# Performance work log

Hardware: AMD Instinct MI355X
Metric: run time of the kernel (lower is better)

The kernel has to match this reference:

```python
import jax, jax.numpy as jnp
import numpy as np
from jax import lax

B, N, C = 16, 2048, 128
NPOINT = 512
RADII = (0.1, 0.2, 0.4)
NSAMPLES = (16, 32, 48)
C_IN = C + 3          # use_xyz: relative xyz concatenated to features
C_OUT = 128
C_MID = C_OUT // 4    # mapping_func1 out channels (non-first-layer)


def fps(xyz, npoint):
    # sequential furthest point sampling; first index is 0 (matches CUDA FPS)
    b, n, _ = xyz.shape
    def step(carry, _):
        dist, last = carry
        p = xyz[jnp.arange(b), last]                    # (B,3) last selected point
        d = jnp.sum((xyz - p[:, None, :]) ** 2, -1)     # (B,N)
        dist = jnp.minimum(dist, d)
        nxt = jnp.argmax(dist, -1).astype(jnp.int32)
        return (dist, nxt), nxt
    idx0 = jnp.zeros((b,), jnp.int32)
    (_, _), rest = lax.scan(step, (jnp.full((b, n), 1e10, jnp.float32), idx0), None, length=npoint - 1)
    return jnp.concatenate([idx0[None], rest], 0).T     # (B,npoint)


def ball_query(xyz, new_xyz, radius, nsample):
    # first `nsample` in-ball indices (in original point order), pad with first hit
    n = xyz.shape[1]
    d2 = jnp.sum((new_xyz[:, :, None, :] - xyz[:, None, :, :]) ** 2, -1)  # (B,np,N)
    scores = jnp.where(d2 < radius * radius, jnp.arange(n, dtype=jnp.int32), n)
    vals = -lax.top_k(-scores, nsample)[0]               # ascending valid indices, invalid == n
    first = vals[..., :1]                                # center is always in its own ball
    return jnp.where(vals >= n, first, vals)             # (B,np,ns) int32


def gather_points(pts, idx):
    # pts (B,N,D), idx (B,np,ns) -> (B,np,ns,D)
    return jax.vmap(lambda p, i: p[i])(pts, idx)


def sa_forward(xyz, features, W1, b1, W2, b2, Wcr, bcr):
    fi = fps(xyz, NPOINT)
    new_xyz = jax.vmap(lambda p, i: p[i])(xyz, fi)       # (B,np,3)
    featT = jnp.transpose(features, (0, 2, 1))           # (B,N,C)
    outs = []
    for r, ns in zip(RADII, NSAMPLES):
        idx = ball_query(xyz, new_xyz, r, ns)
        g_xyz = gather_points(xyz, idx)                  # (B,np,ns,3) absolute neighbor coords
        rel = g_xyz - new_xyz[:, :, None, :]             # relative coords
        gf = gather_points(featT, idx)                   # (B,np,ns,C)
        x = jnp.concatenate([rel, gf], -1)               # (B,np,ns,C_in)
        dist = jnp.linalg.norm(rel, axis=-1, keepdims=True)
        ci = jnp.broadcast_to(new_xyz[:, :, None, :], g_xyz.shape)
        h10 = jnp.concatenate([dist, ci, g_xyz, rel], -1)        # relation prior (B,np,ns,10)
        h = jax.nn.relu(h10 @ W1 + b1) @ W2 + b2                 # dynamic weights (B,np,ns,C_in)
        pooled = jnp.max(jax.nn.relu(h * x), 2)                  # (B,np,C_in) max over neighbors
        outs.append(jax.nn.relu(pooled @ Wcr + bcr))             # channel raising (B,np,C_out)
    new_features = jnp.transpose(jnp.concatenate(outs, -1), (0, 2, 1))  # (B, 3*C_out, np)
    return new_xyz, new_features


def setup_inputs() -> dict:
    key = jax.random.key(0)
    ks = jax.random.split(key, 6)
    s = 0.05
    xyz = jax.random.uniform(ks[0], (B, N, 3), jnp.float32)
    features = jax.random.normal(ks[1], (B, C, N), jnp.float32)
    W1 = jax.random.normal(ks[2], (10, C_MID), jnp.float32) * s
    b1 = jnp.zeros((C_MID,), jnp.float32)
    W2 = jax.random.normal(ks[3], (C_MID, C_IN), jnp.float32) * s
    b2 = jnp.zeros((C_IN,), jnp.float32)
    Wcr = jax.random.normal(ks[4], (C_IN, C_OUT), jnp.float32) * s
    bcr = jnp.zeros((C_OUT,), jnp.float32)
    return dict(xyz=xyz, features=features, W1=W1, b1=b1, W2=W2, b2=b2, Wcr=Wcr, bcr=bcr)


def reference(xyz, features, W1, b1, W2, b2, Wcr, bcr):
    return sa_forward(xyz, features, W1, b1, W2, b2, Wcr, bcr)
```

## Files before the change

kernel.cpp:

```cpp
#include <hip/hip_runtime.h>
#include <hip/hip_bf16.h>

#define BATCH   16
#define NPTS    2048
#define NPOINT  512
#define CFEAT   128
#define CIN     131
#define CMID    32
#define NS_TOT  96

typedef float v2f __attribute__((ext_vector_type(2)));

__device__ __forceinline__ float d2_rn(float ax, float ay, float az,
                                       float bx, float by, float bz) {
  float dx = __fsub_rn(ax, bx), dy = __fsub_rn(ay, by), dz = __fsub_rn(az, bz);
  return __fadd_rn(__fadd_rn(__fmul_rn(dx, dx), __fmul_rn(dy, dy)), __fmul_rn(dz, dz));
}

__device__ __forceinline__ unsigned long long wave_kmax64(unsigned long long k) {
#define KSTEP(CTRL, RMASK, BMASK)                                              \
  {                                                                            \
    unsigned hi = (unsigned)(k >> 32), lo = (unsigned)k;                       \
    unsigned thi = (unsigned)__builtin_amdgcn_update_dpp(                      \
        (int)hi, (int)hi, CTRL, RMASK, BMASK, false);                          \
    unsigned tlo = (unsigned)__builtin_amdgcn_update_dpp(                      \
        (int)lo, (int)lo, CTRL, RMASK, BMASK, false);                          \
    unsigned long long tk = ((unsigned long long)thi << 32) | tlo;             \
    k = tk > k ? tk : k;                                                       \
  }
  KSTEP(0x111, 0xf, 0xf)
  KSTEP(0x112, 0xf, 0xf)
  KSTEP(0x114, 0xf, 0xe)
  KSTEP(0x118, 0xf, 0xc)
  KSTEP(0x142, 0xa, 0xf)
  KSTEP(0x143, 0xc, 0xf)
#undef KSTEP
  return k;
}

__global__ __launch_bounds__(256) void fps_transpose_kernel(
    const float* __restrict__ xyz, const float* __restrict__ feat,
    float* __restrict__ featT, float* __restrict__ out_xyz)
{
  int t = threadIdx.x;
  if (blockIdx.x >= BATCH) {
    __shared__ float tile[32][33];
    int m  = blockIdx.x - BATCH;
    int b  = m >> 8;
    int c0 = ((m >> 6) & 3) << 5;
    int n0 = (m & 63) << 5;
    int tx = t & 31, ty = t >> 5;
    const float* src = feat  + (size_t)b * CFEAT * NPTS;
    float*       dst = featT + (size_t)b * NPTS * CFEAT;
#pragma unroll
    for (int i = 0; i < 4; ++i)
      tile[ty + 8 * i][tx] = src[(size_t)(c0 + ty + 8 * i) * NPTS + n0 + tx];
    __syncthreads();
#pragma unroll
    for (int i = 0; i < 4; ++i)
      dst[(size_t)(n0 + ty + 8 * i) * CFEAT + c0 + tx] = tile[tx][ty + 8 * i];
    return;
  }
  __shared__ float4 sp[NPTS];
  __shared__ unsigned long long skey[2][4];
  __shared__ int slast[NPOINT];
  int b = blockIdx.x;
  const float* xb = xyz + (size_t)b * NPTS * 3;
  for (int n = t; n < NPTS; n += 256) {
    const float* p = xb + n * 3;
    sp[n] = make_float4(p[0], p[1], p[2], 0.f);
  }
  if (t == 0) slast[0] = 0;
  __syncthreads();
  float lx[8], ly[8], lz[8], d[8];
#pragma unroll
  for (int i = 0; i < 8; ++i) {
    float4 q = sp[(i << 8) + t];
    lx[i] = q.x; ly[i] = q.y; lz[i] = q.z;
    d[i] = 1e10f;
  }
  int last = 0;
  int w = t >> 6;
  int tb = 0xFFF - t;
#pragma unroll 1
  for (int step = 1; step < NPOINT; ++step) {
    float4 pv = sp[last];
    unsigned long long best = 0ull;
#pragma unroll
    for (int i = 0; i < 8; ++i) {
      float dd = d2_rn(lx[i], ly[i], lz[i], pv.x, pv.y, pv.z);
      float nd = fminf(d[i], dd);
      d[i] = nd;
      unsigned long long k = ((unsigned long long)__float_as_uint(nd) << 32)
                           | (unsigned)(tb - (i << 8));
      best = (k > best) ? k : best;
    }
    unsigned long long wk = wave_kmax64(best);
    int par = step & 1;
    if ((t & 63) == 63) skey[par][w] = wk;
    __syncthreads();
    unsigned long long k0 = skey[par][0], k1 = skey[par][1];
    unsigned long long k2 = skey[par][2], k3 = skey[par][3];
    unsigned long long ka = k0 > k1 ? k0 : k1;
    unsigned long long kb = k2 > k3 ? k2 : k3;
    unsigned long long km = ka > kb ? ka : kb;
    last = (0xFFF - (int)((unsigned)km & 0xFFFu)) & (NPTS - 1);
    if (t == 0) slast[step] = last;
  }
  __syncthreads();
  for (int s = t; s < NPOINT; s += 256) {
    float4 q = sp[slast[s]];
    float* o = out_xyz + ((size_t)b * NPOINT + s) * 3;
    o[0] = q.x; o[1] = q.y; o[2] = q.z;
  }
}

__global__ __launch_bounds__(128, 4) void center_kernel(
    const float* __restrict__ xyz, const float* __restrict__ featT,
    const float* __restrict__ W1, const float* __restrict__ b1,
    const float* __restrict__ W2, const float* __restrict__ b2,
    const float* __restrict__ Wcr, const float* __restrict__ bcr,
    const float* __restrict__ new_xyz, float* __restrict__ out_feat,
    float* __restrict__ out_tmp)
{
  int j = blockIdx.x, b = blockIdx.y, t = threadIdx.x;
  __shared__ int   sIdx[NS_TOT];
  __shared__ __align__(16) float sH1[NS_TOT * 36];
  __shared__ float sVr[NS_TOT * 4];
  __shared__ __align__(16) float sPooled[3 * 132];

  float cx = new_xyz[((size_t)b * NPOINT + j) * 3 + 0];
  float cy = new_xyz[((size_t)b * NPOINT + j) * 3 + 1];
  float cz = new_xyz[((size_t)b * NPOINT + j) * 3 + 2];

  {
    int w = t >> 6, lane = t & 63;
    const float* xb = xyz + (size_t)b * NPTS * 3;
    unsigned long long lt = (1ull << lane) - 1ull;
    if (w == 0) {
      int c0 = 0, c1 = 0;
      for (int it = 0; it < 32; ++it) {
        int n = (it << 6) + lane;
        float px = xb[n * 3 + 0], py = xb[n * 3 + 1], pz = xb[n * 3 + 2];
        float d2 = d2_rn(cx, cy, cz, px, py, pz);
        bool i0 = d2 < 0.01f, i1 = d2 < 0.04f;
        unsigned long long m0 = __ballot(i0), m1 = __ballot(i1);
        if (i0) { int pos = c0 + __popcll(m0 & lt); if (pos < 16) sIdx[pos] = n; }
        if (i1) { int pos = c1 + __popcll(m1 & lt); if (pos < 32) sIdx[16 + pos] = n; }
        c0 += __popcll(m0); c1 += __popcll(m1);
        if (c0 >= 16 && c1 >= 32) break;
      }
      int f0 = sIdx[0];
      int f1 = sIdx[16];
      if (lane >= c0 && lane < 16) sIdx[lane] = f0;
      if (lane >= c1 && lane < 32) sIdx[16 + lane] = f1;
    } else {
      int c2 = 0;
      for (int it = 0; it < 32; ++it) {
        int n = (it << 6) + lane;
        float px = xb[n * 3 + 0], py = xb[n * 3 + 1], pz = xb[n * 3 + 2];
        float d2 = d2_rn(cx, cy, cz, px, py, pz);
        bool i2 = d2 < 0.16f;
        unsigned long long m2 = __ballot(i2);
        if (i2) { int pos = c2 + __popcll(m2 & lt); if (pos < 48) sIdx[48 + pos] = n; }
        c2 += __popcll(m2);
        if (c2 >= 48) break;
      }
      int f2 = sIdx[48];
      if (lane >= c2 && lane < 48) sIdx[48 + lane] = f2;
    }
  }
  __syncthreads();

  if (t < NS_TOT) {
    int idx = sIdx[t];
    const float* p = xyz + ((size_t)b * NPTS + (size_t)idx) * 3;
    float px = p[0], py = p[1], pz = p[2];
    float rx = __fsub_rn(px, cx), ry = __fsub_rn(py, cy), rz = __fsub_rn(pz, cz);
    float dist = sqrtf(__fadd_rn(__fadd_rn(__fmul_rn(rx, rx), __fmul_rn(ry, ry)),
                                 __fmul_rn(rz, rz)));
    float h10[10] = {dist, cx, cy, cz, px, py, pz, rx, ry, rz};
    float h1r[CMID];
#pragma unroll
    for (int m = 0; m < CMID / 2; ++m) {
      v2f a = { b1[2 * m], b1[2 * m + 1] };
#pragma unroll
      for (int i = 0; i < 10; ++i) {
        v2f wv = { W1[i * CMID + 2 * m], W1[i * CMID + 2 * m + 1] };
        v2f hv = { h10[i], h10[i] };
        a = __builtin_elementwise_fma(hv, wv, a);
      }
      v2f z = { 0.f, 0.f };
      a = __builtin_elementwise_max(a, z);
      h1r[2 * m] = a.x; h1r[2 * m + 1] = a.y;
    }
#pragma unroll
    for (int q = 0; q < 8; ++q)
      *(float4*)&sH1[t * 36 + 4 * q] = *(const float4*)&h1r[4 * q];
    v2f pa0 = { b2[0], 0.f }, pa1 = { b2[1], 0.f }, pa2 = { b2[2], 0.f };
#pragma unroll
    for (int m = 0; m < CMID / 2; ++m) {
      v2f hv = { h1r[2 * m], h1r[2 * m + 1] };
      v2f w0 = { W2[(2 * m) * CIN + 0], W2[(2 * m + 1) * CIN + 0] };
      v2f w1 = { W2[(2 * m) * CIN + 1], W2[(2 * m + 1) * CIN + 1] };
      v2f w2 = { W2[(2 * m) * CIN + 2], W2[(2 * m + 1) * CIN + 2] };
      pa0 = __builtin_elementwise_fma(hv, w0, pa0);
      pa1 = __builtin_elementwise_fma(hv, w1, pa1);
      pa2 = __builtin_elementwise_fma(hv, w2, pa2);
    }
    float a0 = __fadd_rn(pa0.x, pa0.y);
    float a1 = __fadd_rn(pa1.x, pa1.y);
    float a2 = __fadd_rn(pa2.x, pa2.y);
    sVr[t * 4 + 0] = fmaxf(__fmul_rn(a0, rx), 0.f);
    sVr[t * 4 + 1] = fmaxf(__fmul_rn(a1, ry), 0.f);
    sVr[t * 4 + 2] = fmaxf(__fmul_rn(a2, rz), 0.f);
  }
  __syncthreads();

  {
    int w = t >> 6, lane = t & 63;
    v2f wA[16], wB[16];
#pragma unroll
    for (int m = 0; m < 16; ++m) {
      wA[m] = (v2f){ W2[(2 * m) * CIN + 3 + lane],
                     W2[(2 * m + 1) * CIN + 3 + lane] };
      wB[m] = (v2f){ W2[(2 * m) * CIN + 3 + lane + 64],
                     W2[(2 * m + 1) * CIN + 3 + lane + 64] };
    }
    float bA = b2[3 + lane], bB = b2[3 + lane + 64];
    const float* ftb = featT + (size_t)b * NPTS * CFEAT;
    int sBeg = w ? 48 : 0;
    int sEnd = w ? 96 : 48;
    int sMid = w ? 10000 : 16;
    float xA0 = ftb[(size_t)sIdx[sBeg] * CFEAT + lane];
    float xB0 = ftb[(size_t)sIdx[sBeg] * CFEAT + lane + 64];
    float xA1 = ftb[(size_t)sIdx[sBeg + 1] * CFEAT + lane];
    float xB1 = ftb[(size_t)sIdx[sBeg + 1] * CFEAT + lane + 64];
    float plA = 0.f, plB = 0.f;
#pragma unroll 2
    for (int s = sBeg; s < sEnd; ++s) {
      int sp2 = (s + 2 < sEnd) ? s + 2 : sEnd - 1;
      float xA2 = ftb[(size_t)sIdx[sp2] * CFEAT + lane];
      float xB2 = ftb[(size_t)sIdx[sp2] * CFEAT + lane + 64];
      const float4* h4 = (const float4*)&sH1[s * 36];
      v2f aAA = (v2f){ bA, 0.f }, aAB = (v2f){ 0.f, 0.f };
      v2f aBA = (v2f){ bB, 0.f }, aBB = (v2f){ 0.f, 0.f };
#pragma unroll
      for (int q = 0; q < 8; ++q) {
        float4 h = h4[q];
        v2f hxy = (v2f){ h.x, h.y }, hzw = (v2f){ h.z, h.w };
        aAA = __builtin_elementwise_fma(hxy, wA[2 * q],     aAA);
        aAB = __builtin_elementwise_fma(hzw, wA[2 * q + 1], aAB);
        aBA = __builtin_elementwise_fma(hxy, wB[2 * q],     aBA);
        aBB = __builtin_elementwise_fma(hzw, wB[2 * q + 1], aBB);
      }
      float hA = __fadd_rn(__fadd_rn(aAA.x, aAA.y), __fadd_rn(aAB.x, aAB.y));
      float hB = __fadd_rn(__fadd_rn(aBA.x, aBA.y), __fadd_rn(aBB.x, aBB.y));
      plA = fmaxf(plA, fmaxf(__fmul_rn(hA, xA0), 0.f));
      plB = fmaxf(plB, fmaxf(__fmul_rn(hB, xB0), 0.f));
      xA0 = xA1; xA1 = xA2; xB0 = xB1; xB1 = xB2;
      if (s + 1 == sMid) {
        sPooled[0 * 132 + 3 + lane]      = plA;
        sPooled[0 * 132 + 3 + lane + 64] = plB;
        plA = 0.f; plB = 0.f;
      }
    }
    int rowL = w ? 2 : 1;
    sPooled[rowL * 132 + 3 + lane]      = plA;
    sPooled[rowL * 132 + 3 + lane + 64] = plB;
  }
  if (t < 9) {
    int r = t / 3, c = t - r * 3;
    int s0 = (r == 0) ? 0 : (r == 1 ? 16 : 48);
    int s1 = (r == 0) ? 16 : (r == 1 ? 48 : 96);
    float pl = 0.f;
    for (int s = s0; s < s1; ++s) pl = fmaxf(pl, sVr[s * 4 + c]);
    sPooled[r * 132 + c] = pl;
  }
  __syncthreads();

  v2f s01 = { bcr[t], bcr[t] };
  float s2 = bcr[t];
#pragma unroll 2
  for (int k4 = 0; k4 < 128; k4 += 4) {
    float4 p0 = *(const float4*)&sPooled[k4];
    float4 p1 = *(const float4*)&sPooled[132 + k4];
    float4 p2 = *(const float4*)&sPooled[264 + k4];
#pragma unroll
    for (int u = 0; u < 4; ++u) {
      float w = Wcr[(k4 + u) * CFEAT + t];
      float e0 = (&p0.x)[u], e1 = (&p1.x)[u], e2 = (&p2.x)[u];
      s01 = __builtin_elementwise_fma((v2f){ e0, e1 }, (v2f){ w, w }, s01);
      s2  = fmaf(e2, w, s2);
    }
  }
#pragma unroll
  for (int k = 128; k < CIN; ++k) {
    float w = Wcr[k * CFEAT + t];
    s01 = __builtin_elementwise_fma((v2f){ sPooled[k], sPooled[132 + k] },
                                    (v2f){ w, w }, s01);
    s2  = fmaf(sPooled[264 + k], w, s2);
  }
  if (out_tmp) {
    float* ob = out_tmp + ((size_t)b * NPOINT + j) * 384;
    ob[t]       = fmaxf(s01.x, 0.f);
    ob[128 + t] = fmaxf(s01.y, 0.f);
    ob[256 + t] = fmaxf(s2, 0.f);
  } else {
    float* ob = out_feat + (size_t)b * 384 * NPOINT + j;
    ob[(size_t)(0 * CFEAT + t) * NPOINT] = fmaxf(s01.x, 0.f);
    ob[(size_t)(1 * CFEAT + t) * NPOINT] = fmaxf(s01.y, 0.f);
    ob[(size_t)(2 * CFEAT + t) * NPOINT] = fmaxf(s2, 0.f);
  }
}

__global__ __launch_bounds__(256) void untranspose_kernel(
    const float* __restrict__ tmp, float* __restrict__ out_feat)
{
  __shared__ float tile[32][33];
  int jt = blockIdx.x, ct = blockIdx.y, b = blockIdx.z;
  int t = threadIdx.x, tx = t & 31, ty = t >> 5;
  const float* src = tmp      + (size_t)b * NPOINT * 384;
  float*       dst = out_feat + (size_t)b * 384 * NPOINT;
#pragma unroll
  for (int i = 0; i < 4; ++i)
    tile[ty + 8 * i][tx] = src[(size_t)(jt * 32 + ty + 8 * i) * 384 + ct * 32 + tx];
  __syncthreads();
#pragma unroll
  for (int i = 0; i < 4; ++i)
    dst[(size_t)(ct * 32 + ty + 8 * i) * NPOINT + jt * 32 + tx] = tile[tx][ty + 8 * i];
}

extern "C" void kernel_launch(void* const* d_in, const int* in_sizes, int n_in,
                              void* d_out, int out_size, void* d_ws, size_t ws_size,
                              hipStream_t stream) {
  const float* xyz  = (const float*)d_in[0];
  const float* feat = (const float*)d_in[1];
  const float* W1   = (const float*)d_in[2];
  const float* b1   = (const float*)d_in[3];
  const float* W2   = (const float*)d_in[4];
  const float* b2   = (const float*)d_in[5];
  const float* Wcr  = (const float*)d_in[6];
  const float* bcr  = (const float*)d_in[7];
  float* out_xyz  = (float*)d_out;
  float* out_feat = out_xyz + (size_t)BATCH * NPOINT * 3;
  float* featT    = (float*)d_ws;
  size_t featT_bytes = (size_t)BATCH * NPTS * CFEAT * sizeof(float);
  size_t tmp_bytes   = (size_t)BATCH * NPOINT * 384 * sizeof(float);

  fps_transpose_kernel<<<BATCH + BATCH * 256, 256, 0, stream>>>(xyz, feat, featT, out_xyz);

  if (ws_size >= featT_bytes + tmp_bytes) {
    float* tmp = (float*)((char*)d_ws + featT_bytes);
    center_kernel<<<dim3(NPOINT, BATCH), 128, 0, stream>>>(
        xyz, featT, W1, b1, W2, b2, Wcr, bcr, (const float*)d_out, out_feat, tmp);
    untranspose_kernel<<<dim3(NPOINT / 32, 384 / 32, BATCH), 256, 0, stream>>>(
        tmp, out_feat);
  } else {
    center_kernel<<<dim3(NPOINT, BATCH), 128, 0, stream>>>(
        xyz, featT, W1, b1, W2, b2, Wcr, bcr, (const float*)d_out, out_feat, nullptr);
  }
}
```

Measured before the change: 488.5 us.

## Run FPS on a single wavefront to drop per-step block barriers

The furthest-point-sampling loop now runs on only the first 64 threads, each holding 32 points in packed float2 registers. The per-step shared-memory key exchange and __syncthreads are replaced by a wave-level DPP reduction plus readlane, which removes block-wide synchronisation from each of the 511 sequential steps. In exchange, each thread does four times more distance work per step, so the serial chain per step grows; packed v2f math is meant to offset that. Argmax tie-breaking is kept by comparing float bits first and index second.

```diff
diff --git a/kernel.cpp b/kernel.cpp
--- a/kernel.cpp
+++ b/kernel.cpp
@@ -62,7 +62,6 @@
     return;
   }
   __shared__ float4 sp[NPTS];
-  __shared__ unsigned long long skey[2][4];
   __shared__ int slast[NPOINT];
   int b = blockIdx.x;
   const float* xb = xyz + (size_t)b * NPTS * 3;
@@ -72,43 +71,52 @@
   }
   if (t == 0) slast[0] = 0;
   __syncthreads();
-  float lx[8], ly[8], lz[8], d[8];
-#pragma unroll
-  for (int i = 0; i < 8; ++i) {
-    float4 q = sp[(i << 8) + t];
-    lx[i] = q.x; ly[i] = q.y; lz[i] = q.z;
-    d[i] = 1e10f;
-  }
-  int last = 0;
-  int w = t >> 6;
-  int tb = 0xFFF - t;
+  if (t >= 64) return;
+
+  v2f plx[16], ply[16], plz[16], dv[16];
+#pragma unroll
+  for (int k = 0; k < 16; ++k) {
+    float4 q0 = sp[((2 * k) << 6) + t];
+    float4 q1 = sp[((2 * k + 1) << 6) + t];
+    plx[k] = (v2f){ q0.x, q1.x };
+    ply[k] = (v2f){ q0.y, q1.y };
+    plz[k] = (v2f){ q0.z, q1.z };
+    dv[k]  = (v2f){ 1e10f, 1e10f };
+  }
+  float4 p0v = sp[0];
+  float pvx = p0v.x, pvy = p0v.y, pvz = p0v.z;
+  unsigned tb = 0xFFFu - (unsigned)t;
 #pragma unroll 1
   for (int step = 1; step < NPOINT; ++step) {
-    float4 pv = sp[last];
-    unsigned long long best = 0ull;
-#pragma unroll
-    for (int i = 0; i < 8; ++i) {
-      float dd = d2_rn(lx[i], ly[i], lz[i], pv.x, pv.y, pv.z);
-      float nd = fminf(d[i], dd);
-      d[i] = nd;
-      unsigned long long k = ((unsigned long long)__float_as_uint(nd) << 32)
-                           | (unsigned)(tb - (i << 8));
-      best = (k > best) ? k : best;
-    }
+    unsigned bestu = 0u; unsigned bi = tb;
+    {
+#pragma clang fp contract(off)
+      v2f pvx2 = (v2f){ pvx, pvx };
+      v2f pvy2 = (v2f){ pvy, pvy };
+      v2f pvz2 = (v2f){ pvz, pvz };
+#pragma unroll
+      for (int k = 0; k < 16; ++k) {
+        v2f dx = plx[k] - pvx2;
+        v2f dy = ply[k] - pvy2;
+        v2f dz = plz[k] - pvz2;
+        v2f dd = dx * dx + dy * dy + dz * dz;
+        v2f nd = __builtin_elementwise_min(dv[k], dd);
+        dv[k] = nd;
+        unsigned u0 = __float_as_uint(nd.x);
+        unsigned u1 = __float_as_uint(nd.y);
+        if (u0 > bestu) { bestu = u0; bi = tb - (unsigned)((2 * k) << 6); }
+        if (u1 > bestu) { bestu = u1; bi = tb - (unsigned)((2 * k + 1) << 6); }
+      }
+    }
+    unsigned long long best = ((unsigned long long)bestu << 32) | bi;
     unsigned long long wk = wave_kmax64(best);
-    int par = step & 1;
-    if ((t & 63) == 63) skey[par][w] = wk;
-    __syncthreads();
-    unsigned long long k0 = skey[par][0], k1 = skey[par][1];
-    unsigned long long k2 = skey[par][2], k3 = skey[par][3];
-    unsigned long long ka = k0 > k1 ? k0 : k1;
-    unsigned long long kb = k2 > k3 ? k2 : k3;
-    unsigned long long km = ka > kb ? ka : kb;
-    last = (0xFFF - (int)((unsigned)km & 0xFFFu)) & (NPTS - 1);
+    unsigned lo63 = (unsigned)__builtin_amdgcn_readlane((int)(unsigned)wk, 63);
+    int last = (int)((0xFFFu - (lo63 & 0xFFFu)) & (NPTS - 1));
+    float4 q = sp[last];
+    pvx = q.x; pvy = q.y; pvz = q.z;
     if (t == 0) slast[step] = last;
   }
-  __syncthreads();
-  for (int s = t; s < NPOINT; s += 256) {
+  for (int s = t; s < NPOINT; s += 64) {
     float4 q = sp[slast[s]];
     float* o = out_xyz + ((size_t)b * NPOINT + s) * 3;
     o[0] = q.x; o[1] = q.y; o[2] = q.z;
```

Result: slower. 597.7 us (+22.3%).
